# Performance work log

Measured on AMD Instinct MI355X. Metric: run time of the kernel, lower is better.

## Reference

```python
import jax, jax.numpy as jnp
import numpy as np
from jax import lax

DEPTH = 8
D_MODEL = 768
D_INNER = 2 * D_MODEL      # 1536
D_STATE = 16
DT_RANK = 48               # ceil(768/16)
D_CONV = 4
PATCH = 64
IN_CH = 3
IMG_H, IMG_W = 1280, 960
GRID = ((IMG_H - PATCH) // PATCH + 1, (IMG_W - PATCH) // PATCH + 1)  # (20,15)
NUM_PATCHES = GRID[0] * GRID[1]  # 300
MID = NUM_PATCHES // 2           # middle cls-token position
L = NUM_PATCHES + 1              # 301
EPS = 1e-5


def rmsnorm(x, w):
    return x * lax.rsqrt(jnp.mean(x * x, axis=-1, keepdims=True) + EPS) * w


def dwconv_causal(u, w, b):
    # u: (B,L,C), w: (C,k) depthwise, b: (C,) -- causal conv along L
    C = u.shape[-1]
    k = w.shape[-1]
    up = jnp.pad(u, ((0, 0), (k - 1, 0), (0, 0)))
    out = lax.conv_general_dilated(
        up.transpose(0, 2, 1), w[:, None, :], (1,), 'VALID',
        dimension_numbers=('NCH', 'OIH', 'NCH'), feature_group_count=C)
    return out.transpose(0, 2, 1) + b


def ssm_branch(u, convw, convb, Wx, Wdt, bdt, Alog, Dskip):
    # u: (B,L,d_inner) -> selective state-space scan output (B,L,d_inner)
    uc = jax.nn.silu(dwconv_causal(u, convw, convb))
    x_dbl = jnp.einsum('bld,ed->ble', uc, Wx)              # (B,L,dr+2*ds)
    dt, Bm, Cm = jnp.split(x_dbl, [DT_RANK, DT_RANK + D_STATE], axis=-1)
    delta = jax.nn.softplus(jnp.einsum('blr,dr->bld', dt, Wdt) + bdt)  # (B,L,di)
    A = -jnp.exp(Alog)                                     # (di, ds)

    def step(h, inp):
        d_t, B_t, C_t, u_t = inp                           # (B,di),(B,ds),(B,ds),(B,di)
        dA = jnp.exp(d_t[:, :, None] * A)                  # (B,di,ds)
        dBu = d_t[:, :, None] * B_t[:, None, :] * u_t[:, :, None]
        h = dA * h + dBu
        y = jnp.einsum('bds,bs->bd', h, C_t)
        return h, y

    Bsz = u.shape[0]
    h0 = jnp.zeros((Bsz, D_INNER, D_STATE), dtype=u.dtype)
    seq = (delta.transpose(1, 0, 2), Bm.transpose(1, 0, 2),
           Cm.transpose(1, 0, 2), uc.transpose(1, 0, 2))
    _, ys = lax.scan(step, h0, seq)
    return ys.transpose(1, 0, 2) + uc * Dskip


def _forward(x, patch_w, patch_b, cls_token, pos_embed, norm_ws,
             Win, convw_f, convb_f, Wx_f, Wdt_f, bdt_f, Alog_f, Dskip_f,
             convw_b, convb_b, Wx_b, Wdt_b, bdt_b, Alog_b, Dskip_b,
             Wout, normf_w):
    B = x.shape[0]
    # patch embed: Conv2d(3->768, k=64, s=64)
    feat = lax.conv_general_dilated(
        x, patch_w, (PATCH, PATCH), 'VALID',
        dimension_numbers=('NCHW', 'OIHW', 'NCHW')) + patch_b[None, :, None, None]
    tok = feat.reshape(B, D_MODEL, NUM_PATCHES).transpose(0, 2, 1)  # (B,300,768)
    cls = jnp.broadcast_to(cls_token, (B, 1, D_MODEL))
    tokens = jnp.concatenate([tok[:, :MID], cls, tok[:, MID:]], axis=1) + pos_embed

    def layer_step(carry, p):
        (nw, W_in, cwf, cbf, Wxf, Wdtf, bdtf, Alf, Df,
         cwb, cbb, Wxb, Wdtb, bdtb, Alb, Db, W_out) = p
        hidden, residual = carry
        residual = residual + hidden
        h = rmsnorm(residual, nw)
        xz = jnp.einsum('bld,ed->ble', h, W_in)            # (B,L,2*di)
        xs, z = jnp.split(xz, 2, axis=-1)
        yf = ssm_branch(xs, cwf, cbf, Wxf, Wdtf, bdtf, Alf, Df)
        yb = ssm_branch(xs[:, ::-1], cwb, cbb, Wxb, Wdtb, bdtb, Alb, Db)[:, ::-1]
        y = (yf + yb) * jax.nn.silu(z)
        out = jnp.einsum('ble,de->bld', y, W_out) / 2.0    # if_divide_out=True
        return (out, residual), None

    params = (norm_ws, Win, convw_f, convb_f, Wx_f, Wdt_f, bdt_f, Alog_f, Dskip_f,
              convw_b, convb_b, Wx_b, Wdt_b, bdt_b, Alog_b, Dskip_b, Wout)
    (hidden, residual), _ = lax.scan(
        layer_step, (tokens, jnp.zeros_like(tokens)), params)
    return rmsnorm(residual + hidden, normf_w)


def setup_inputs() -> dict:
    key = jax.random.key(0)
    ks = jax.random.split(key, 24)
    B = 2
    s = 0.02
    inv_sp = float(np.log(np.expm1(0.01)))  # softplus^-1(0.01)
    inp = {
        'x': jax.random.normal(ks[0], (B, IN_CH, IMG_H, IMG_W), jnp.float32),
        'patch_w': jax.random.normal(ks[1], (D_MODEL, IN_CH, PATCH, PATCH), jnp.float32) * s,
        'patch_b': jnp.zeros((D_MODEL,), jnp.float32),
        'cls_token': jax.random.normal(ks[2], (1, 1, D_MODEL), jnp.float32) * s,
        'pos_embed': jax.random.normal(ks[3], (1, L, D_MODEL), jnp.float32) * s,
        'norm_ws': jnp.ones((DEPTH, D_MODEL), jnp.float32),
        'Win': jax.random.normal(ks[4], (DEPTH, 2 * D_INNER, D_MODEL), jnp.float32) * s,
        'convw_f': jax.random.normal(ks[5], (DEPTH, D_INNER, D_CONV), jnp.float32) * 0.2,
        'convb_f': jnp.zeros((DEPTH, D_INNER), jnp.float32),
        'Wx_f': jax.random.normal(ks[6], (DEPTH, DT_RANK + 2 * D_STATE, D_INNER), jnp.float32) * s,
        'Wdt_f': jax.random.normal(ks[7], (DEPTH, D_INNER, DT_RANK), jnp.float32) * 0.1,
        'bdt_f': jnp.full((DEPTH, D_INNER), inv_sp, jnp.float32),
        'Alog_f': jnp.broadcast_to(jnp.log(jnp.arange(1, D_STATE + 1, dtype=jnp.float32)), (DEPTH, D_INNER, D_STATE)).copy(),
        'Dskip_f': jnp.ones((DEPTH, D_INNER), jnp.float32),
        'convw_b': jax.random.normal(ks[8], (DEPTH, D_INNER, D_CONV), jnp.float32) * 0.2,
        'convb_b': jnp.zeros((DEPTH, D_INNER), jnp.float32),
        'Wx_b': jax.random.normal(ks[9], (DEPTH, DT_RANK + 2 * D_STATE, D_INNER), jnp.float32) * s,
        'Wdt_b': jax.random.normal(ks[10], (DEPTH, D_INNER, DT_RANK), jnp.float32) * 0.1,
        'bdt_b': jnp.full((DEPTH, D_INNER), inv_sp, jnp.float32),
        'Alog_b': jnp.broadcast_to(jnp.log(jnp.arange(1, D_STATE + 1, dtype=jnp.float32)), (DEPTH, D_INNER, D_STATE)).copy(),
        'Dskip_b': jnp.ones((DEPTH, D_INNER), jnp.float32),
        'Wout': jax.random.normal(ks[11], (DEPTH, D_MODEL, D_INNER), jnp.float32) * s,
        'normf_w': jnp.ones((D_MODEL,), jnp.float32),
    }
    return inp


def reference(x, patch_w, patch_b, cls_token, pos_embed, norm_ws,
              Win, convw_f, convb_f, Wx_f, Wdt_f, bdt_f, Alog_f, Dskip_f,
              convw_b, convb_b, Wx_b, Wdt_b, bdt_b, Alog_b, Dskip_b,
              Wout, normf_w):
    return _forward(x, patch_w, patch_b, cls_token, pos_embed, norm_ws,
                    Win, convw_f, convb_f, Wx_f, Wdt_f, bdt_f, Alog_f, Dskip_f,
                    convw_b, convb_b, Wx_b, Wdt_b, bdt_b, Alog_b, Dskip_b,
                    Wout, normf_w)
```

## Files before the change

### kernel.cpp

```cpp
#include <hip/hip_runtime.h>
#include <hip/hip_bf16.h>
#include <math.h>

typedef unsigned short ushort_t;
typedef __attribute__((ext_vector_type(8))) short bf16x8;
typedef __attribute__((ext_vector_type(4))) float f32x4;

#define B_    2
#define L_    301
#define MID_  150
#define DM_   768
#define DI_   1536
#define DS_   16
#define DR_   48
#define XD_   80
#define NP_   300
#define EPS_  1e-5f
#define TP_   40

__device__ __forceinline__ float bf2f(ushort_t u) {
  union { float f; unsigned int i; } v; v.i = ((unsigned int)u) << 16; return v.f;
}
__device__ __forceinline__ ushort_t f2bf(float f) {
  __hip_bfloat16 h = __float2bfloat16(f);
  return *reinterpret_cast<ushort_t*>(&h);
}
__device__ __forceinline__ float silu_f(float x) { return x / (1.f + __expf(-x)); }
__device__ __forceinline__ float softplus_f(float x) {
  return fmaxf(x, 0.f) + log1pf(__expf(-fabsf(x)));
}

__device__ __forceinline__ float ld1(const void* p, size_t i, int bf) {
  if (bf) return bf2f(((const ushort_t*)p)[i]);
  return ((const float*)p)[i];
}
__device__ __forceinline__ float4 ld4(const void* p, size_t i, int bf) {
  if (bf) {
    uint2 r = *(const uint2*)((const ushort_t*)p + i);
    return make_float4(bf2f((ushort_t)(r.x & 0xffffu)), bf2f((ushort_t)(r.x >> 16)),
                       bf2f((ushort_t)(r.y & 0xffffu)), bf2f((ushort_t)(r.y >> 16)));
  }
  return *(const float4*)((const float*)p + i);
}

__global__ void detect_dtype(const unsigned int* __restrict__ w, int* __restrict__ flag) {
  *flag = (w[0] == 0x3F803F80u) ? 1 : 0;
}

__global__ __launch_bounds__(256) void gemm64(
    const void* A0, const void* A1, int abf, int lda,
    const void* W0, const void* W1, size_t Woff,
    void* C0, void* C1, int cbf, int ldc,
    const void* bias0, const void* bias1, size_t boff,
    int M, int N, int K, int kc_len, int nbr,
    int mode, float scale,
    const ushort_t* gyf0, const ushort_t* gyb0, const ushort_t* gz,
    const int* __restrict__ dflag)
{
  const int bf = *dflag;
  const int br = blockIdx.z % nbr;
  const int kc = blockIdx.z / nbr;
  const void* A = br ? A1 : A0;
  const void* W = br ? W1 : W0;
  void* C = br ? C1 : C0;
  const void* bias = br ? bias1 : bias0;

  __shared__ ushort_t sA[64 * TP_];
  __shared__ ushort_t sW[64 * TP_];

  const int m0 = blockIdx.x * 64, n0 = blockIdx.y * 64;
  const int t = threadIdx.x;
  const int lane = t & 63, wave = t >> 6;
  const int l16 = lane & 15, quad = lane >> 4;
  const int srow = t >> 2, scol = (t & 3) * 8;

  const int gm = m0 + srow;
  size_t grb = 0, grbrev = 0;
  if (gyf0 && gm < M) {
    int gb = gm / L_, gl = gm % L_;
    grb = (size_t)(gb * L_ + gl);
    grbrev = (size_t)(gb * L_ + (L_ - 1 - gl));
  }

  f32x4 acc[4];
#pragma unroll
  for (int i = 0; i < 4; ++i) acc[i] = (f32x4){0.f, 0.f, 0.f, 0.f};

  const int kstart = kc * kc_len;
  const int kend = (kstart + kc_len < K) ? (kstart + kc_len) : K;

  ushort_t tA[8] __attribute__((aligned(16)));
  ushort_t tW[8] __attribute__((aligned(16)));

  auto stageA = [&](int k0) {
    int m = m0 + srow;
    if (m < M) {
      if (gyf0) {
#pragma unroll
        for (int q = 0; q < 8; q += 4) {
          int k = k0 + scol + q;
          if (k + 4 <= kend) {
            float4 vf = ld4(gyf0, grb * DI_ + k, 1);
            float4 vb = ld4(gyb0, grbrev * DI_ + k, 1);
            float4 vz = ld4(gz, grb * (2 * DI_) + DI_ + k, 1);
            tA[q+0] = f2bf((vf.x + vb.x) * silu_f(vz.x));
            tA[q+1] = f2bf((vf.y + vb.y) * silu_f(vz.y));
            tA[q+2] = f2bf((vf.z + vb.z) * silu_f(vz.z));
            tA[q+3] = f2bf((vf.w + vb.w) * silu_f(vz.w));
          } else { tA[q+0]=0; tA[q+1]=0; tA[q+2]=0; tA[q+3]=0; }
        }
      } else {
#pragma unroll
        for (int q = 0; q < 8; q += 4) {
          int k = k0 + scol + q;
          float4 v = (k + 4 <= kend) ? ld4(A, (size_t)m * lda + k, abf)
                                     : make_float4(0.f, 0.f, 0.f, 0.f);
          tA[q+0]=f2bf(v.x); tA[q+1]=f2bf(v.y); tA[q+2]=f2bf(v.z); tA[q+3]=f2bf(v.w);
        }
      }
    } else {
#pragma unroll
      for (int q = 0; q < 8; ++q) tA[q] = 0;
    }
  };
  auto stageW = [&](int k0) {
    int n = n0 + srow;
    if (n < N) {
#pragma unroll
      for (int q = 0; q < 8; q += 4) {
        int k = k0 + scol + q;
        float4 v = (k + 4 <= kend) ? ld4(W, Woff + (size_t)n * K + k, bf)
                                   : make_float4(0.f, 0.f, 0.f, 0.f);
        tW[q+0]=f2bf(v.x); tW[q+1]=f2bf(v.y); tW[q+2]=f2bf(v.z); tW[q+3]=f2bf(v.w);
      }
    } else {
#pragma unroll
      for (int q = 0; q < 8; ++q) tW[q] = 0;
    }
  };

  stageA(kstart); stageW(kstart);
  for (int k0 = kstart; k0 < kend; k0 += 32) {
    *(uint4*)&sA[srow * TP_ + scol] = *(const uint4*)tA;
    *(uint4*)&sW[srow * TP_ + scol] = *(const uint4*)tW;
    __syncthreads();
    int kn = k0 + 32;
    if (kn >= kend) kn = kstart;
    stageA(kn); stageW(kn);
    bf16x8 bw = *(const bf16x8*)&sW[(wave * 16 + l16) * TP_ + quad * 8];
#pragma unroll
    for (int i = 0; i < 4; ++i) {
      bf16x8 af = *(const bf16x8*)&sA[(i * 16 + l16) * TP_ + quad * 8];
      acc[i] = __builtin_amdgcn_mfma_f32_16x16x32_bf16(af, bw, acc[i], 0, 0, 0);
    }
    __syncthreads();
  }

  int n = n0 + wave * 16 + l16;
  if (n < N) {
    float bval = (mode == 1) ? ld1(bias, boff + n, bf) : 0.f;
#pragma unroll
    for (int i = 0; i < 4; ++i) {
#pragma unroll
      for (int r = 0; r < 4; ++r) {
        int m = m0 + i * 16 + quad * 4 + r;
        if (m >= M) continue;
        float v = acc[i][r] * scale;
        if (mode == 1) v = softplus_f(v + bval);
        if (mode == 2) atomicAdd((float*)C + (size_t)m * ldc + n, v);
        else if (cbf)  ((ushort_t*)C)[(size_t)m * ldc + n] = f2bf(v);
        else           ((float*)C)[(size_t)m * ldc + n] = v;
      }
    }
  }
}

__global__ __launch_bounds__(256) void gemm_patch_mfma(
    const void* __restrict__ X, const void* __restrict__ Wp,
    float* __restrict__ rawp, const int* __restrict__ dflag)
{
  const int bf = *dflag;
  __shared__ ushort_t sA[64 * TP_];
  __shared__ ushort_t sW[128 * TP_];

  const int m0 = blockIdx.x * 64, n0 = blockIdx.y * 128;
  const int kbase = blockIdx.z * 512;
  const int t = threadIdx.x;
  const int lane = t & 63, wave = t >> 6;
  const int l16 = lane & 15, quad = lane >> 4;

  const int srowA = t >> 2, scolA = (t & 3) * 8;
  const int srowW = t >> 1, scolW = (t & 1) * 16;

  const int m = m0 + srowA;
  const int bb = m / NP_, p = m % NP_;
  const int ph = p / 15, pw = p % 15;
  const bool mok = (m < 600);

  f32x4 acc[4][2];
#pragma unroll
  for (int i = 0; i < 4; ++i)
#pragma unroll
    for (int j = 0; j < 2; ++j) acc[i][j] = (f32x4){0.f, 0.f, 0.f, 0.f};

  ushort_t tA[8] __attribute__((aligned(16)));
  ushort_t tW[16] __attribute__((aligned(16)));

  auto stageA = [&](int kc) {
    if (mok) {
      int k = kbase + kc + scolA;
      int c = k >> 12, ky = (k >> 6) & 63, kx = k & 63;
      size_t xi = ((size_t)((bb * 3 + c) * 1280 + ph * 64 + ky)) * 960 + pw * 64 + kx;
#pragma unroll
      for (int q = 0; q < 8; q += 4) {
        float4 v = ld4(X, xi + q, bf);
        tA[q+0]=f2bf(v.x); tA[q+1]=f2bf(v.y); tA[q+2]=f2bf(v.z); tA[q+3]=f2bf(v.w);
      }
    } else {
#pragma unroll
      for (int q = 0; q < 8; ++q) tA[q] = 0;
    }
  };
  auto stageW = [&](int kc) {
    int n = n0 + srowW;
    size_t wb = (size_t)n * 12288 + kbase + kc + scolW;
#pragma unroll
    for (int q = 0; q < 16; q += 4) {
      float4 v = ld4(Wp, wb + q, bf);
      tW[q+0]=f2bf(v.x); tW[q+1]=f2bf(v.y); tW[q+2]=f2bf(v.z); tW[q+3]=f2bf(v.w);
    }
  };

  stageA(0); stageW(0);
  for (int kc = 0; kc < 512; kc += 32) {
    *(uint4*)&sA[srowA * TP_ + scolA] = *(const uint4*)tA;
    *(uint4*)&sW[srowW * TP_ + scolW]     = *(const uint4*)&tW[0];
    *(uint4*)&sW[srowW * TP_ + scolW + 8] = *(const uint4*)&tW[8];
    __syncthreads();
    int kn = (kc + 32 < 512) ? kc + 32 : 0;
    stageA(kn); stageW(kn);

    bf16x8 af[4], bw[2];
#pragma unroll
    for (int i = 0; i < 4; ++i)
      af[i] = *(const bf16x8*)&sA[(i * 16 + l16) * TP_ + quad * 8];
#pragma unroll
    for (int j = 0; j < 2; ++j)
      bw[j] = *(const bf16x8*)&sW[(wave * 32 + j * 16 + l16) * TP_ + quad * 8];
#pragma unroll
    for (int i = 0; i < 4; ++i)
#pragma unroll
      for (int j = 0; j < 2; ++j)
        acc[i][j] = __builtin_amdgcn_mfma_f32_16x16x32_bf16(af[i], bw[j], acc[i][j], 0, 0, 0);
    __syncthreads();
  }

#pragma unroll
  for (int i = 0; i < 4; ++i) {
#pragma unroll
    for (int r = 0; r < 4; ++r) {
      int mm = m0 + i * 16 + quad * 4 + r;
      if (mm >= 600) continue;
#pragma unroll
      for (int j = 0; j < 2; ++j) {
        int nn = n0 + wave * 32 + j * 16 + l16;
        atomicAdd(&rawp[(size_t)mm * DM_ + nn], acc[i][j][r]);
      }
    }
  }
}

__global__ void assemble_tokens(const float* __restrict__ rawp,
                                const void* __restrict__ patch_b,
                                const void* __restrict__ cls,
                                const void* __restrict__ pos,
                                float* __restrict__ hidden, float* __restrict__ residual,
                                const int* __restrict__ dflag)
{
  const int bf = *dflag;
  int idx = blockIdx.x * 256 + threadIdx.x;
  int d = idx % DM_;
  int bl = idx / DM_;
  int l = bl % L_;
  int b = bl / L_;
  float v;
  if (l == MID_) v = ld1(cls, d, bf);
  else {
    int pp = (l < MID_) ? l : l - 1;
    v = ld1(patch_b, d, bf) + rawp[(size_t)(b * NP_ + pp) * DM_ + d];
  }
  v += ld1(pos, (size_t)l * DM_ + d, bf);
  hidden[idx] = v;
  residual[idx] = 0.f;
}

__global__ __launch_bounds__(256) void prenorm_rms(
    float* __restrict__ residual, const float* __restrict__ hidden,
    const void* __restrict__ nw, size_t nwoff, ushort_t* __restrict__ hn,
    const int* __restrict__ dflag)
{
  const int bf = *dflag;
  const int row = blockIdx.x;
  const int t = threadIdx.x;
  const size_t base = (size_t)row * DM_;
  float v[3];
  float ss = 0.f;
#pragma unroll
  for (int i = 0; i < 3; ++i) {
    int c = t + i * 256;
    float x = residual[base + c] + hidden[base + c];
    v[i] = x;
    residual[base + c] = x;
    ss += x * x;
  }
#pragma unroll
  for (int off = 32; off > 0; off >>= 1) ss += __shfl_down(ss, off);
  __shared__ float ps[4];
  if ((t & 63) == 0) ps[t >> 6] = ss;
  __syncthreads();
  float rs = rsqrtf((ps[0] + ps[1] + ps[2] + ps[3]) / (float)DM_ + EPS_);
#pragma unroll
  for (int i = 0; i < 3; ++i) {
    int c = t + i * 256;
    hn[base + c] = f2bf(v[i] * rs * ld1(nw, nwoff + c, bf));
  }
}

__global__ void conv_silu(const ushort_t* __restrict__ xz,
                          const void* __restrict__ cwf, const void* __restrict__ cbf,
                          const void* __restrict__ cwb, const void* __restrict__ cbb,
                          size_t cwoff, size_t cboff,
                          ushort_t* __restrict__ ucf, ushort_t* __restrict__ ucb,
                          float* __restrict__ xdz,
                          const int* __restrict__ dflag)
{
  const int bf = *dflag;
  int idx = blockIdx.x * 256 + threadIdx.x;
  if (idx < 96320) xdz[idx] = 0.f;
  int d = idx % DI_;
  int bl = idx / DI_;
  int l = bl % L_;
  int b = bl / L_;
  float af = ld1(cbf, cboff + d, bf);
#pragma unroll
  for (int k = 0; k < 4; ++k) {
    int lo = l - 3 + k;
    if (lo >= 0) af += ld1(cwf, cwoff + d * 4 + k, bf) * bf2f(xz[((size_t)(b * L_ + lo)) * (2*DI_) + d]);
  }
  ucf[idx] = f2bf(silu_f(af));
  float ab = ld1(cbb, cboff + d, bf);
#pragma unroll
  for (int k = 0; k < 4; ++k) {
    int j = l - 3 + k;
    if (j >= 0) ab += ld1(cwb, cwoff + d * 4 + k, bf) * bf2f(xz[((size_t)(b * L_ + (L_ - 1 - j))) * (2*DI_) + d]);
  }
  ucb[idx] = f2bf(silu_f(ab));
}

__global__ __launch_bounds__(256) void scan_kernel(
    const ushort_t* __restrict__ uc0, ushort_t* dl0, const float* __restrict__ xd0,
    const ushort_t* __restrict__ uc1, ushort_t* dl1, const float* __restrict__ xd1,
    const void* __restrict__ Al_f, const void* __restrict__ Dk_f,
    const void* __restrict__ Al_b, const void* __restrict__ Dk_b,
    size_t Aoff, size_t Doff, float* __restrict__ hidz,
    const int* __restrict__ dflag)
{
  const int bf = *dflag;
  const int b = blockIdx.y;
  const int br = blockIdx.z;

  {
    int gtid = (blockIdx.x + 24 * (blockIdx.y + 2 * blockIdx.z)) * 256 + threadIdx.x;
    for (int i = gtid; i < B_ * L_ * DM_; i += 96 * 256) hidz[i] = 0.f;
  }

  const ushort_t* uc = br ? uc1 : uc0;
  ushort_t* dl = br ? dl1 : dl0;
  const float* xd = br ? xd1 : xd0;
  const void* Al = br ? Al_b : Al_f;
  const void* Dk = br ? Dk_b : Dk_f;

  __shared__ float sBC[L_ * 32];
  for (int i = threadIdx.x; i < L_ * 8; i += 256) {
    int l = i >> 3, q = i & 7;
    *(float4*)&sBC[l * 32 + q * 4] = *(const float4*)&xd[(size_t)(b * L_ + l) * XD_ + DR_ + q * 4];
  }
  __syncthreads();

  const int ch = threadIdx.x >> 2;
  const int sl = threadIdx.x & 3;
  const int d = blockIdx.x * 64 + ch;
  float Areg[4], h[4];
#pragma unroll
  for (int s = 0; s < 4; ++s) {
    Areg[s] = -__expf(ld1(Al, Aoff + (size_t)d * 16 + sl * 4 + s, bf));
    h[s] = 0.f;
  }
  const float Dsk = ld1(Dk, Doff + d, bf);

  size_t idx = (size_t)(b * L_) * DI_ + d;
  float dt = bf2f(dl[idx]);
  float u  = bf2f(uc[idx]);
  for (int l = 0; l < L_; ++l) {
    float dtn = 0.f, un = 0.f;
    if (l + 1 < L_) {
      dtn = bf2f(dl[idx + DI_]);
      un  = bf2f(uc[idx + DI_]);
    }
    const float* bc = &sBC[l * 32 + sl * 4];
    float du = dt * u;
    float yv = 0.f;
#pragma unroll
    for (int s = 0; s < 4; ++s) {
      float dA = __expf(dt * Areg[s]);
      h[s] = dA * h[s] + du * bc[s];
      yv += h[s] * bc[16 + s];
    }
    yv += __shfl_xor(yv, 1);
    yv += __shfl_xor(yv, 2);
    dl[idx] = f2bf(yv + u * Dsk);
    dt = dtn; u = un; idx += DI_;
  }
}

__global__ __launch_bounds__(256) void final_norm(
    const float* __restrict__ residual, const float* __restrict__ hidden,
    const void* __restrict__ nfw, void* __restrict__ out,
    const int* __restrict__ dflag)
{
  const int bf = *dflag;
  const int row = blockIdx.x;
  const int t = threadIdx.x;
  const size_t base = (size_t)row * DM_;
  float v[3];
  float ss = 0.f;
#pragma unroll
  for (int i = 0; i < 3; ++i) {
    int c = t + i * 256;
    float x = residual[base + c] + hidden[base + c];
    v[i] = x;
    ss += x * x;
  }
#pragma unroll
  for (int off = 32; off > 0; off >>= 1) ss += __shfl_down(ss, off);
  __shared__ float ps[4];
  if ((t & 63) == 0) ps[t >> 6] = ss;
  __syncthreads();
  float rs = rsqrtf((ps[0] + ps[1] + ps[2] + ps[3]) / (float)DM_ + EPS_);
#pragma unroll
  for (int i = 0; i < 3; ++i) {
    int c = t + i * 256;
    float val = v[i] * rs * ld1(nfw, c, bf);
    if (bf) ((__hip_bfloat16*)out)[base + c] = __float2bfloat16(val);
    else    ((float*)out)[base + c] = val;
  }
}

extern "C" void kernel_launch(void* const* d_in, const int* in_sizes, int n_in,
                              void* d_out, int out_size, void* d_ws, size_t ws_size,
                              hipStream_t stream)
{
  const void* X        = d_in[0];
  const void* patch_w  = d_in[1];
  const void* patch_b  = d_in[2];
  const void* cls      = d_in[3];
  const void* pos      = d_in[4];
  const void* norm_ws  = d_in[5];
  const void* Win      = d_in[6];
  const void* convw_f  = d_in[7];
  const void* convb_f  = d_in[8];
  const void* Wx_f     = d_in[9];
  const void* Wdt_f    = d_in[10];
  const void* bdt_f    = d_in[11];
  const void* Alog_f   = d_in[12];
  const void* Dskip_f  = d_in[13];
  const void* convw_b  = d_in[14];
  const void* convb_b  = d_in[15];
  const void* Wx_b     = d_in[16];
  const void* Wdt_b    = d_in[17];
  const void* bdt_b    = d_in[18];
  const void* Alog_b   = d_in[19];
  const void* Dskip_b  = d_in[20];
  const void* Wout     = d_in[21];
  const void* normf_w  = d_in[22];

  const int BL = B_ * L_;

  char* base = (char*)d_ws;
  int*      dflag    = (int*)(base + 0);
  float*    hidden   = (float*)(base + 256);
  float*    residual = (float*)(base + 1849600);
  ushort_t* hn       = (ushort_t*)(base + 3698944);
  ushort_t* xz       = (ushort_t*)(base + 4623616);
  ushort_t* ucf      = (ushort_t*)(base + 8322304);
  ushort_t* ucb      = (ushort_t*)(base + 10171648);
  ushort_t* dlf      = (ushort_t*)(base + 12020992);
  ushort_t* dlb      = (ushort_t*)(base + 13870336);
  float*    xdf      = (float*)(base + 15719680);
  float*    xdb      = (float*)(base + 15912320);
  float*    rawp     = (float*)(base + 4623616);
  ushort_t* yf       = dlf;
  ushort_t* yb       = dlb;

  detect_dtype<<<1, 1, 0, stream>>>((const unsigned int*)norm_ws, dflag);

  hipMemsetAsync(rawp, 0, 600 * DM_ * 4, stream);
  gemm_patch_mfma<<<dim3(10, 6, 24), 256, 0, stream>>>(X, patch_w, rawp, dflag);
  assemble_tokens<<<(BL * DM_) / 256, 256, 0, stream>>>(rawp, patch_b, cls, pos, hidden, residual, dflag);

  for (int layer = 0; layer < 8; ++layer) {
    size_t nwoff   = (size_t)layer * DM_;
    size_t Winoff  = (size_t)layer * 2 * DI_ * DM_;
    size_t cwoff   = (size_t)layer * DI_ * 4;
    size_t cboff   = (size_t)layer * DI_;
    size_t Wxoff   = (size_t)layer * XD_ * DI_;
    size_t Wdtoff  = (size_t)layer * DI_ * DR_;
    size_t bdtoff  = (size_t)layer * DI_;
    size_t Aloff   = (size_t)layer * DI_ * DS_;
    size_t Dkoff   = (size_t)layer * DI_;
    size_t Woutoff = (size_t)layer * DM_ * DI_;

    prenorm_rms<<<BL, 256, 0, stream>>>(residual, hidden, norm_ws, nwoff, hn, dflag);

    gemm64<<<dim3(10, 48, 1), 256, 0, stream>>>(
        hn, hn, 1, DM_, Win, Win, Winoff, xz, xz, 1, 2 * DI_,
        nullptr, nullptr, 0, BL, 2 * DI_, DM_, DM_, 1, 0, 1.f,
        nullptr, nullptr, nullptr, dflag);

    conv_silu<<<(BL * DI_) / 256, 256, 0, stream>>>(xz, convw_f, convb_f, convw_b, convb_b,
                                                    cwoff, cboff, ucf, ucb, xdf, dflag);

    gemm64<<<dim3(10, 2, 16), 256, 0, stream>>>(
        ucf, ucb, 1, DI_, Wx_f, Wx_b, Wxoff, xdf, xdb, 0, XD_,
        nullptr, nullptr, 0, BL, XD_, DI_, 192, 2, 2, 1.f,
        nullptr, nullptr, nullptr, dflag);

    gemm64<<<dim3(10, 24, 2), 256, 0, stream>>>(
        xdf, xdb, 0, XD_, Wdt_f, Wdt_b, Wdtoff, dlf, dlb, 1, DI_,
        bdt_f, bdt_b, bdtoff, BL, DI_, DR_, DR_, 2, 1, 1.f,
        nullptr, nullptr, nullptr, dflag);

    scan_kernel<<<dim3(24, 2, 2), 256, 0, stream>>>(ucf, dlf, xdf, ucb, dlb, xdb,
                                                    Alog_f, Dskip_f, Alog_b, Dskip_b,
                                                    Aloff, Dkoff, hidden, dflag);

    gemm64<<<dim3(10, 12, 4), 256, 0, stream>>>(
        dlf, dlf, 1, DI_, Wout, Wout, Woutoff, hidden, hidden, 0, DM_,
        nullptr, nullptr, 0, BL, DM_, DI_, 384, 1, 2, 0.5f,
        yf, yb, xz, dflag);
  }

  final_norm<<<BL, 256, 0, stream>>>(residual, hidden, normf_w, d_out, dflag);
}
```

Baseline: 1.735 ms.

## Fuse RMSNorm into in_proj GEMM and delta projection into scan kernel

Drops the separate prenorm kernel. The in_proj GEMM now computes each row's RMS scale itself and applies the norm weight while staging A. Residual and hidden are merged into one buffer that out_proj accumulates into atomically, which removes the zeroing done inside the scan. The dt projection plus softplus moves into the scan kernel as an MFMA into shared memory, which removes one GEMM launch and the delta round trip through global memory. The patch GEMM uses a longer K chunk per block with fewer z-splits. In exchange, every in_proj block redundantly recomputes the row norms and the scan uses far more shared memory, which may lower occupancy.

```diff
diff --git a/kernel.cpp b/kernel.cpp
--- a/kernel.cpp
+++ b/kernel.cpp
@@ -55,6 +55,7 @@
     int M, int N, int K, int kc_len, int nbr,
     int mode, float scale,
     const ushort_t* gyf0, const ushort_t* gyb0, const ushort_t* gz,
+    const void* nwp, size_t nwoff,
     const int* __restrict__ dflag)
 {
   const int bf = *dflag;
@@ -80,6 +81,22 @@
     int gb = gm / L_, gl = gm % L_;
     grb = (size_t)(gb * L_ + gl);
     grbrev = (size_t)(gb * L_ + (L_ - 1 - gl));
+  }
+
+  float s_scale = 0.f;
+  if (nwp) {
+    float ss = 0.f;
+    if (gm < M) {
+      const float* ar = (const float*)A + (size_t)gm * lda;
+      for (int j = (t & 3) * 4; j < K; j += 16) {
+        float4 v = *(const float4*)&ar[j];
+        ss = fmaf(v.x, v.x, ss); ss = fmaf(v.y, v.y, ss);
+        ss = fmaf(v.z, v.z, ss); ss = fmaf(v.w, v.w, ss);
+      }
+    }
+    ss += __shfl_xor(ss, 1);
+    ss += __shfl_xor(ss, 2);
+    s_scale = rsqrtf(ss / (float)K + EPS_);
   }
 
   f32x4 acc[4];
@@ -109,6 +126,18 @@
             tA[q+3] = f2bf((vf.w + vb.w) * silu_f(vz.w));
           } else { tA[q+0]=0; tA[q+1]=0; tA[q+2]=0; tA[q+3]=0; }
         }
+      } else if (nwp) {
+#pragma unroll
+        for (int q = 0; q < 8; q += 4) {
+          int k = k0 + scol + q;
+          if (k + 4 <= kend) {
+            float4 v = *(const float4*)((const float*)A + (size_t)m * lda + k);
+            tA[q+0] = f2bf(v.x * s_scale * ld1(nwp, nwoff + k + 0, bf));
+            tA[q+1] = f2bf(v.y * s_scale * ld1(nwp, nwoff + k + 1, bf));
+            tA[q+2] = f2bf(v.z * s_scale * ld1(nwp, nwoff + k + 2, bf));
+            tA[q+3] = f2bf(v.w * s_scale * ld1(nwp, nwoff + k + 3, bf));
+          } else { tA[q+0]=0; tA[q+1]=0; tA[q+2]=0; tA[q+3]=0; }
+        }
       } else {
 #pragma unroll
         for (int q = 0; q < 8; q += 4) {
@@ -184,7 +213,7 @@
   __shared__ ushort_t sW[128 * TP_];
 
   const int m0 = blockIdx.x * 64, n0 = blockIdx.y * 128;
-  const int kbase = blockIdx.z * 512;
+  const int kbase = blockIdx.z * 1024;
   const int t = threadIdx.x;
   const int lane = t & 63, wave = t >> 6;
   const int l16 = lane & 15, quad = lane >> 4;
@@ -232,12 +261,12 @@
   };
 
   stageA(0); stageW(0);
-  for (int kc = 0; kc < 512; kc += 32) {
+  for (int kc = 0; kc < 1024; kc += 32) {
     *(uint4*)&sA[srowA * TP_ + scolA] = *(const uint4*)tA;
     *(uint4*)&sW[srowW * TP_ + scolW]     = *(const uint4*)&tW[0];
     *(uint4*)&sW[srowW * TP_ + scolW + 8] = *(const uint4*)&tW[8];
     __syncthreads();
-    int kn = (kc + 32 < 512) ? kc + 32 : 0;
+    int kn = (kc + 32 < 1024) ? kc + 32 : 0;
     stageA(kn); stageW(kn);
 
     bf16x8 af[4], bw[2];
@@ -274,7 +303,7 @@
                                 const void* __restrict__ patch_b,
                                 const void* __restrict__ cls,
                                 const void* __restrict__ pos,
-                                float* __restrict__ hidden, float* __restrict__ residual,
+                                float* __restrict__ residual,
                                 const int* __restrict__ dflag)
 {
   const int bf = *dflag;
@@ -290,40 +319,7 @@
     v = ld1(patch_b, d, bf) + rawp[(size_t)(b * NP_ + pp) * DM_ + d];
   }
   v += ld1(pos, (size_t)l * DM_ + d, bf);
-  hidden[idx] = v;
-  residual[idx] = 0.f;
-}
-
-__global__ __launch_bounds__(256) void prenorm_rms(
-    float* __restrict__ residual, const float* __restrict__ hidden,
-    const void* __restrict__ nw, size_t nwoff, ushort_t* __restrict__ hn,
-    const int* __restrict__ dflag)
-{
-  const int bf = *dflag;
-  const int row = blockIdx.x;
-  const int t = threadIdx.x;
-  const size_t base = (size_t)row * DM_;
-  float v[3];
-  float ss = 0.f;
-#pragma unroll
-  for (int i = 0; i < 3; ++i) {
-    int c = t + i * 256;
-    float x = residual[base + c] + hidden[base + c];
-    v[i] = x;
-    residual[base + c] = x;
-    ss += x * x;
-  }
-#pragma unroll
-  for (int off = 32; off > 0; off >>= 1) ss += __shfl_down(ss, off);
-  __shared__ float ps[4];
-  if ((t & 63) == 0) ps[t >> 6] = ss;
-  __syncthreads();
-  float rs = rsqrtf((ps[0] + ps[1] + ps[2] + ps[3]) / (float)DM_ + EPS_);
-#pragma unroll
-  for (int i = 0; i < 3; ++i) {
-    int c = t + i * 256;
-    hn[base + c] = f2bf(v[i] * rs * ld1(nw, nwoff + c, bf));
-  }
+  residual[idx] = v;
 }
 
 __global__ void conv_silu(const ushort_t* __restrict__ xz,
@@ -358,37 +354,82 @@
 }
 
 __global__ __launch_bounds__(256) void scan_kernel(
-    const ushort_t* __restrict__ uc0, ushort_t* dl0, const float* __restrict__ xd0,
-    const ushort_t* __restrict__ uc1, ushort_t* dl1, const float* __restrict__ xd1,
+    const ushort_t* __restrict__ uc0, ushort_t* __restrict__ dl0, const float* __restrict__ xd0,
+    const ushort_t* __restrict__ uc1, ushort_t* __restrict__ dl1, const float* __restrict__ xd1,
     const void* __restrict__ Al_f, const void* __restrict__ Dk_f,
     const void* __restrict__ Al_b, const void* __restrict__ Dk_b,
-    size_t Aoff, size_t Doff, float* __restrict__ hidz,
+    const void* __restrict__ Wdt_f, const void* __restrict__ Wdt_b,
+    const void* __restrict__ bdt_f, const void* __restrict__ bdt_b,
+    size_t Aoff, size_t Doff, size_t Wdtoff, size_t bdtoff,
     const int* __restrict__ dflag)
 {
   const int bf = *dflag;
   const int b = blockIdx.y;
   const int br = blockIdx.z;
-
-  {
-    int gtid = (blockIdx.x + 24 * (blockIdx.y + 2 * blockIdx.z)) * 256 + threadIdx.x;
-    for (int i = gtid; i < B_ * L_ * DM_; i += 96 * 256) hidz[i] = 0.f;
-  }
-
   const ushort_t* uc = br ? uc1 : uc0;
   ushort_t* dl = br ? dl1 : dl0;
   const float* xd = br ? xd1 : xd0;
   const void* Al = br ? Al_b : Al_f;
   const void* Dk = br ? Dk_b : Dk_f;
-
+  const void* Wd = br ? Wdt_b : Wdt_f;
+  const void* bd = br ? bdt_b : bdt_f;
+
+  __shared__ ushort_t sXD[304 * 72];
+  __shared__ ushort_t sDL[304 * 72];
   __shared__ float sBC[L_ * 32];
-  for (int i = threadIdx.x; i < L_ * 8; i += 256) {
+
+  const int t = threadIdx.x;
+  for (int i = t; i < 304 * 8; i += 256) {
+    int l = i >> 3, q = i & 7;
+    ushort_t tmp[8] __attribute__((aligned(16)));
+#pragma unroll
+    for (int j = 0; j < 8; ++j) {
+      int c = q * 8 + j;
+      float v = (l < L_ && c < DR_) ? xd[(size_t)(b * L_ + l) * XD_ + c] : 0.f;
+      tmp[j] = f2bf(v);
+    }
+    *(uint4*)&sXD[l * 72 + q * 8] = *(const uint4*)tmp;
+  }
+  for (int i = t; i < L_ * 8; i += 256) {
     int l = i >> 3, q = i & 7;
     *(float4*)&sBC[l * 32 + q * 4] = *(const float4*)&xd[(size_t)(b * L_ + l) * XD_ + DR_ + q * 4];
   }
   __syncthreads();
 
-  const int ch = threadIdx.x >> 2;
-  const int sl = threadIdx.x & 3;
+  {
+    const int lane = t & 63, wave = t >> 6;
+    const int l16 = lane & 15, quad = lane >> 4;
+    const int dch = blockIdx.x * 64 + wave * 16 + l16;
+    bf16x8 bwf[2];
+#pragma unroll
+    for (int kk = 0; kk < 2; ++kk) {
+      ushort_t tmp[8] __attribute__((aligned(16)));
+#pragma unroll
+      for (int j = 0; j < 8; ++j) {
+        int r = kk * 32 + quad * 8 + j;
+        tmp[j] = (r < DR_) ? f2bf(ld1(Wd, Wdtoff + (size_t)dch * DR_ + r, bf)) : (ushort_t)0;
+      }
+      bwf[kk] = *(const bf16x8*)tmp;
+    }
+    const float bv = ld1(bd, bdtoff + dch, bf);
+    for (int mt = 0; mt < 19; ++mt) {
+      f32x4 acc = (f32x4){0.f, 0.f, 0.f, 0.f};
+#pragma unroll
+      for (int kk = 0; kk < 2; ++kk) {
+        bf16x8 af = *(const bf16x8*)&sXD[(mt * 16 + l16) * 72 + kk * 32 + quad * 8];
+        acc = __builtin_amdgcn_mfma_f32_16x16x32_bf16(af, bwf[kk], acc, 0, 0, 0);
+      }
+#pragma unroll
+      for (int rr = 0; rr < 4; ++rr) {
+        int row = mt * 16 + quad * 4 + rr;
+        sDL[row * 72 + wave * 16 + l16] = f2bf(softplus_f(acc[rr] + bv));
+      }
+    }
+  }
+  __syncthreads();
+
+  const int ch = t >> 2;
+  const int sl = t & 3;
   const int d = blockIdx.x * 64 + ch;
   float Areg[4], h[4];
 #pragma unroll
@@ -399,12 +440,12 @@
   const float Dsk = ld1(Dk, Doff + d, bf);
 
   size_t idx = (size_t)(b * L_) * DI_ + d;
-  float dt = bf2f(dl[idx]);
+  float dt = bf2f(sDL[ch]);
   float u  = bf2f(uc[idx]);
   for (int l = 0; l < L_; ++l) {
     float dtn = 0.f, un = 0.f;
     if (l + 1 < L_) {
-      dtn = bf2f(dl[idx + DI_]);
+      dtn = bf2f(sDL[(l + 1) * 72 + ch]);
       un  = bf2f(uc[idx + DI_]);
     }
     const float* bc = &sBC[l * 32 + sl * 4];
@@ -424,7 +465,7 @@
 }
 
 __global__ __launch_bounds__(256) void final_norm(
-    const float* __restrict__ residual, const float* __restrict__ hidden,
+    const float* __restrict__ residual,
     const void* __restrict__ nfw, void* __restrict__ out,
     const int* __restrict__ dflag)
 {
@@ -437,7 +478,7 @@
 #pragma unroll
   for (int i = 0; i < 3; ++i) {
     int c = t + i * 256;
-    float x = residual[base + c] + hidden[base + c];
+    float x = residual[base + c];
     v[i] = x;
     ss += x * x;
   }
@@ -488,9 +529,7 @@
 
   char* base = (char*)d_ws;
   int*      dflag    = (int*)(base + 0);
-  float*    hidden   = (float*)(base + 256);
   float*    residual = (float*)(base + 1849600);
-  ushort_t* hn       = (ushort_t*)(base + 3698944);
   ushort_t* xz       = (ushort_t*)(base + 4623616);
   ushort_t* ucf      = (ushort_t*)(base + 8322304);
   ushort_t* ucb      = (ushort_t*)(base + 10171648);
@@ -505,8 +544,8 @@
   detect_dtype<<<1, 1, 0, stream>>>((const unsigned int*)norm_ws, dflag);
 
   hipMemsetAsync(rawp, 0, 600 * DM_ * 4, stream);
-  gemm_patch_mfma<<<dim3(10, 6, 24), 256, 0, stream>>>(X, patch_w, rawp, dflag);
-  assemble_tokens<<<(BL * DM_) / 256, 256, 0, stream>>>(rawp, patch_b, cls, pos, hidden, residual, dflag);
+  gemm_patch_mfma<<<dim3(10, 6, 12), 256, 0, stream>>>(X, patch_w, rawp, dflag);
+  assemble_tokens<<<(BL * DM_) / 256, 256, 0, stream>>>(rawp, patch_b, cls, pos, residual, dflag);
 
   for (int layer = 0; layer < 8; ++layer) {
     size_t nwoff   = (size_t)layer * DM_;
@@ -520,12 +559,10 @@
     size_t Dkoff   = (size_t)layer * DI_;
     size_t Woutoff = (size_t)layer * DM_ * DI_;
 
-    prenorm_rms<<<BL, 256, 0, stream>>>(residual, hidden, norm_ws, nwoff, hn, dflag);
-
     gemm64<<<dim3(10, 48, 1), 256, 0, stream>>>(
-        hn, hn, 1, DM_, Win, Win, Winoff, xz, xz, 1, 2 * DI_,
+        residual, residual, 0, DM_, Win, Win, Winoff, xz, xz, 1, 2 * DI_,
         nullptr, nullptr, 0, BL, 2 * DI_, DM_, DM_, 1, 0, 1.f,
-        nullptr, nullptr, nullptr, dflag);
+        nullptr, nullptr, nullptr, norm_ws, nwoff, dflag);
 
     conv_silu<<<(BL * DI_) / 256, 256, 0, stream>>>(xz, convw_f, convb_f, convw_b, convb_b,
                                                     cwoff, cboff, ucf, ucb, xdf, dflag);
@@ -533,22 +570,18 @@
     gemm64<<<dim3(10, 2, 16), 256, 0, stream>>>(
         ucf, ucb, 1, DI_, Wx_f, Wx_b, Wxoff, xdf, xdb, 0, XD_,
         nullptr, nullptr, 0, BL, XD_, DI_, 192, 2, 2, 1.f,
-        nullptr, nullptr, nullptr, dflag);
-
-    gemm64<<<dim3(10, 24, 2), 256, 0, stream>>>(
-        xdf, xdb, 0, XD_, Wdt_f, Wdt_b, Wdtoff, dlf, dlb, 1, DI_,
-        bdt_f, bdt_b, bdtoff, BL, DI_, DR_, DR_, 2, 1, 1.f,
-        nullptr, nullptr, nullptr, dflag);
+        nullptr, nullptr, nullptr, nullptr, 0, dflag);
 
     scan_kernel<<<dim3(24, 2, 2), 256, 0, stream>>>(ucf, dlf, xdf, ucb, dlb, xdb,
                                                     Alog_f, Dskip_f, Alog_b, Dskip_b,
-                                                    Aloff, Dkoff, hidden, dflag);
+                                                    Wdt_f, Wdt_b, bdt_f, bdt_b,
+                                                    Aloff, Dkoff, Wdtoff, bdtoff, dflag);
 
     gemm64<<<dim3(10, 12, 4), 256, 0, stream>>>(
-        dlf, dlf, 1, DI_, Wout, Wout, Woutoff, hidden, hidden, 0, DM_,
+        dlf, dlf, 1, DI_, Wout, Wout, Woutoff, residual, residual, 0, DM_,
         nullptr, nullptr, 0, BL, DM_, DI_, 384, 1, 2, 0.5f,
-        yf, yb, xz, dflag);
-  }
-
-  final_norm<<<BL, 256, 0, stream>>>(residual, hidden, normf_w, d_out, dflag);
-}
+        yf, yb, xz, nullptr, 0, dflag);
+  }
+
+  final_norm<<<BL, 256, 0, stream>>>(residual, normf_w, d_out, dflag);
+}
```

After: 1.825 ms. 5.2% more time.
